# Kernel optimization log

Measured on AMD Instinct MI355X. Metric: run time of the kernel, lower is better.

## Reference

```python
import jax, jax.numpy as jnp
import numpy as np

N_ATOMS = 4096
BOX = 37.0
CUTOFF = 5.0


def _f_r(r, fe, beta, re, lam):
    # f_e * exp(-beta*(r/r_e - 1)) / (1 + (r/r_e - lamda)^20)
    x = r / re
    return fe * jnp.exp(-beta * (x - 1.0)) / (1.0 + (x - lam) ** 20)


def _phi_r(r, a, b, re, alpha, beta, kappa, lam):
    x = r / re
    l = a * jnp.exp(-alpha * (x - 1.0)) / (1.0 + (x - kappa) ** 20)
    rr = b * jnp.exp(-beta * (x - 1.0)) / (1.0 + (x - lam) ** 20)
    return l - rr


def setup_inputs() -> dict:
    key = jax.random.key(0)
    k1, k2 = jax.random.split(key)
    # coordinates in a box sized for metal-like density so neighbors exist within cutoff
    coords = jax.random.uniform(k1, (N_ATOMS, 3), dtype=jnp.float32) * BOX
    # all 22 EAM parameters positive in [1.0, 2.5] (r_e, rho_s, rho_n, rho_0, eta must be > 0)
    params = 1.0 + 1.5 * jax.random.uniform(k2, (N_ATOMS, 22), dtype=jnp.float32)
    return {"coords": coords, "params": params}


def reference(coords, params):
    N = coords.shape[0]
    # docstring column order: r_e, f_e, rho_e, rho_s, alpha, beta, A, B, kappa, lamda,
    # f_n0..f_n3, f_0..f_3, eta, f_e2, rho_n, rho_0
    r_e, f_e, rho_e, rho_s = params[:, 0], params[:, 1], params[:, 2], params[:, 3]
    alpha, beta = params[:, 4], params[:, 5]
    A, B, kappa, lam = params[:, 6], params[:, 7], params[:, 8], params[:, 9]
    eta, f_e2 = params[:, 18], params[:, 19]
    rho_n, rho_0 = params[:, 20], params[:, 21]

    # ---- full pairwise distances (safe diagonal for differentiable sqrt) ----
    diff = coords[None, :, :] - coords[:, None, :]            # [N, N, 3]
    r2 = jnp.sum(diff * diff, axis=-1)                        # [N, N]
    eye = jnp.eye(N, dtype=bool)
    r_mat = jnp.sqrt(jnp.where(eye, 1.0, r2))                 # [N, N]

    # ---- pair energy over i<j with r <= cutoff (masked, same math as torch filtering) ----
    iu, ju = jnp.triu_indices(N, k=1)                         # P = N(N-1)/2 pairs
    r_pair = r_mat[iu, ju]
    mask = r_pair <= CUTOFF
    r_safe = jnp.where(mask, r_pair, 1.0)                     # nan-safe for masked-out pairs

    fr_i = _f_r(r_safe, f_e[iu], beta[iu], r_e[iu], lam[iu])
    fr_j = _f_r(r_safe, f_e[ju], beta[ju], r_e[ju], lam[ju])
    ph_i = _phi_r(r_safe, A[iu], B[iu], r_e[iu], alpha[iu], beta[iu], kappa[iu], lam[iu])
    ph_j = _phi_r(r_safe, A[ju], B[ju], r_e[ju], alpha[ju], beta[ju], kappa[ju], lam[ju])
    phi_01 = fr_j / fr_i * ph_i + fr_i / fr_j * ph_j
    p_e = 0.5 * jnp.sum(jnp.where(mask, phi_01, 0.0))

    # ---- per-atom density rho_i = sum_{j != i} f_r(r_ij, params_j) (no cutoff, as in source) ----
    fr_mat = _f_r(r_mat, f_e[None, :], beta[None, :], r_e[None, :], lam[None, :])
    rho = jnp.sum(jnp.where(eye, 0.0, fr_mat), axis=1)        # [N]

    # ---- embedding F(rho) with three branches (if/elif/else -> nested where) ----
    xn = rho / rho_n - 1.0
    poly_n = params[:, 10] + params[:, 11] * xn + params[:, 12] * xn ** 2 + params[:, 13] * xn ** 3
    xe = rho / rho_e - 1.0
    poly_0 = params[:, 14] + params[:, 15] * xe + params[:, 16] * xe ** 2 + params[:, 17] * xe ** 3
    t = (rho / rho_s) ** eta
    tail = f_e2 * (1.0 - jnp.log(t)) * t
    F_i = jnp.where(rho < rho_n, poly_n, jnp.where(rho < rho_0, poly_0, tail))

    return p_e + jnp.sum(F_i)
```

## Files before the change

kernel.cpp:

```cpp
#include <hip/hip_runtime.h>
#include <math.h>

#define N_ATOMS 4096
#define NTILE   16
#define NJ      64
#define JT      64
#define LOG2E   1.4426950408889634f
#define LN2     0.6931471805599453f

typedef float v2f __attribute__((ext_vector_type(2)));
typedef unsigned long long u64;

__device__ __forceinline__ float pow20f(float t) {
    float t2 = t * t, t4 = t2 * t2, t8 = t4 * t4, t16 = t8 * t8;
    return t16 * t4;
}

__device__ __forceinline__ float block_reduce(float v, float* red) {
    __syncthreads();
    #pragma unroll
    for (int off = 32; off > 0; off >>= 1) v += __shfl_down(v, off, 64);
    if ((threadIdx.x & 63) == 0) red[threadIdx.x >> 6] = v;
    __syncthreads();
    return (red[0] + red[1]) + (red[2] + red[3]);
}

__global__ __launch_bounds__(256) void pack_kernel(
    const float* __restrict__ coords, const float* __restrict__ params,
    float* __restrict__ apk, float* __restrict__ rpk, int* __restrict__ ctr)
{
    if (blockIdx.x == 0 && threadIdx.x == 0) *ctr = 0;
    const int a = blockIdx.x * 256 + threadIdx.x;
    const float* p = params + 22 * a;
    const float x = coords[3*a], y = coords[3*a+1], z = coords[3*a+2];
    const float re = p[0], fe = p[1], be = p[5], al = p[4], la = p[9];
    const float rei  = __builtin_amdgcn_rcpf(re);
    const float bl2  = be * LOG2E;
    const float al2  = al * LOG2E;
    const float l2fe = __builtin_amdgcn_logf(fe);

    float lo = la + 1.0f, hi = la + 6.0f;
    #pragma unroll 1
    for (int it = 0; it < 28; ++it) {
        const float mid = 0.5f * (lo + hi);
        const float t   = mid - la;
        const float g   = l2fe - bl2 * (mid - 1.0f)
                        - __builtin_amdgcn_logf(1.0f + pow20f(t)) + 19.93f;
        if (g > 0.0f) lo = mid; else hi = mid;
    }
    const float rc  = re * hi;
    const float rc2 = fmaxf(rc * rc, 25.01f);

    float4* ad = (float4*)(apk + 12 * a);
    ad[0] = { x, y, z, rei };
    ad[1] = { -bl2 * rei, bl2 + l2fe, -la, p[7] * __builtin_amdgcn_rcpf(fe) };
    ad[2] = { -al2 * rei, al2, -p[8], p[6] };

    float* rd = rpk + 8 * (a >> 1) + (a & 1);
    rd[0] = x; rd[2] = y; rd[4] = z; rd[6] = rc2;
}

__global__ __launch_bounds__(256) void eam_main(
    const float* __restrict__ apk, const float* __restrict__ rpk,
    float* __restrict__ rho_part,
    float* __restrict__ e_part)
{
    __shared__ float4 srho4[JT];
    __shared__ float4 sphi4[JT * 3];
    __shared__ float red[4];

    const int tid = threadIdx.x;
    const int bi  = blockIdx.x;
    const int s   = blockIdx.y;
    const int i   = bi * 256 + tid;
    const int jbase = s * JT;

    if (tid < JT)       srho4[tid]      = ((const float4*)rpk)[s * JT + tid];
    else                sphi4[tid - 64] = ((const float4*)apk)[s * 192 + (tid - 64)];

    const float4* apk4 = (const float4*)apk;
    const float4 a0 = apk4[i * 3 + 0];
    const float4 a1 = apk4[i * 3 + 1];
    const float4 a2 = apk4[i * 3 + 2];

    __syncthreads();

    const v2f xi2 = { a0.x, a0.x }, yi2 = { a0.y, a0.y }, zi2 = { a0.z, a0.z };
    u64 hits = 0ull;

    #pragma unroll 4
    for (int k = 0; k < JT / 2; ++k) {
        const float4 f0 = srho4[k * 2 + 0];
        const float4 f1 = srho4[k * 2 + 1];
        const v2f x01 = { f0.x, f0.y }, y01 = { f0.z, f0.w };
        const v2f z01 = { f1.x, f1.y };
        const v2f dx = x01 - xi2, dy = y01 - yi2, dz = z01 - zi2;
        const v2f r2v = dx * dx + dy * dy + dz * dz;
        if (r2v.x <= f1.z) hits |= (1ull << (2 * k));
        if (r2v.y <= f1.w) hits |= (1ull << (2 * k + 1));
    }

    const int t = i - jbase;
    float rho = 0.0f;
    u64 phim = 0ull;

    {
        u64 m = hits;
        if (t >= 0 && t < JT) m &= ~(1ull << t);
        while (m) {
            const int k = __builtin_ctzll(m);
            m &= m - 1;
            const float4 q0 = sphi4[k * 3 + 0];
            const float4 q1 = sphi4[k * 3 + 1];
            const float dx = q0.x - a0.x, dy = q0.y - a0.y, dz = q0.z - a0.z;
            const float r2 = fmaf(dx, dx, fmaf(dy, dy, dz * dz));
            const float r  = __builtin_amdgcn_sqrtf(r2);
            const float fr = __builtin_amdgcn_exp2f(fmaf(r, q1.x, q1.y))
                           * __builtin_amdgcn_rcpf(1.0f + pow20f(fmaf(r, q0.w, q1.z)));
            rho += fr;
            if (r2 <= 25.0f && k > t) phim |= (1ull << k);
        }
    }
    rho_part[(size_t)s * N_ATOMS + i] = rho;

    float e = 0.0f;
    while (phim) {
        const int k = __builtin_ctzll(phim);
        phim &= phim - 1;
        const float4 q0 = sphi4[k * 3 + 0];
        const float4 q1 = sphi4[k * 3 + 1];
        const float4 q2 = sphi4[k * 3 + 2];
        const float dx = q0.x - a0.x, dy = q0.y - a0.y, dz = q0.z - a0.z;
        const float r = __builtin_amdgcn_sqrtf(fmaf(dx, dx, fmaf(dy, dy, dz * dz)));

        const float fri = __builtin_amdgcn_exp2f(fmaf(r, a1.x, a1.y))
                        * __builtin_amdgcn_rcpf(1.0f + pow20f(fmaf(r, a0.w, a1.z)));
        const float frj = __builtin_amdgcn_exp2f(fmaf(r, q1.x, q1.y))
                        * __builtin_amdgcn_rcpf(1.0f + pow20f(fmaf(r, q0.w, q1.z)));
        const float ph_i = a2.w * __builtin_amdgcn_exp2f(fmaf(r, a2.x, a2.y))
                                * __builtin_amdgcn_rcpf(1.0f + pow20f(fmaf(r, a0.w, a2.z)))
                         - a1.w * fri;
        const float ph_j = q2.w * __builtin_amdgcn_exp2f(fmaf(r, q2.x, q2.y))
                                * __builtin_amdgcn_rcpf(1.0f + pow20f(fmaf(r, q0.w, q2.z)))
                         - q1.w * frj;
        e += 0.5f * fmaf(frj * frj, ph_i, fri * fri * ph_j)
                  * __builtin_amdgcn_rcpf(fri * frj);
    }

    const float eb = block_reduce(e, red);
    if (tid == 0) e_part[bi * NJ + s] = eb;
}

__global__ __launch_bounds__(1024) void eam_embed(
    const float* __restrict__ params,
    const float* __restrict__ rho_part, const float* __restrict__ e_part,
    float* __restrict__ tile_sum,
    int* __restrict__ ctr, float* __restrict__ out)
{
    __shared__ float acc[4][256];
    __shared__ float red16[16];
    __shared__ int sLast;
    const int tid = threadIdx.x;
    const int b   = blockIdx.x;
    const int al  = tid & 255;
    const int q   = tid >> 8;
    const int i   = b * 256 + al;

    float part = 0.0f;
    #pragma unroll 4
    for (int s = q * 16; s < q * 16 + 16; ++s)
        part += rho_part[(size_t)s * N_ATOMS + i];
    acc[q][al] = part;
    __syncthreads();

    float v = 0.0f;
    if (tid < 256) {
        const float rhoi = (acc[0][tid] + acc[1][tid]) + (acc[2][tid] + acc[3][tid]);
        const float* p = params + 22 * i;
        float F;
        if (rhoi < p[20]) {
            const float xn = rhoi / p[20] - 1.0f;
            F = p[10] + xn * (p[11] + xn * (p[12] + xn * p[13]));
        } else if (rhoi < p[21]) {
            const float xe = rhoi / p[2] - 1.0f;
            F = p[14] + xe * (p[15] + xe * (p[16] + xe * p[17]));
        } else {
            const float l2 = __builtin_amdgcn_logf(rhoi / p[3]);
            const float tt = __builtin_amdgcn_exp2f(p[18] * l2);
            const float lt = p[18] * l2 * LN2;
            F = p[19] * (1.0f - lt) * tt;
        }
        v = F + ((tid < NJ) ? e_part[b * NJ + tid] : 0.0f);
    }

    #pragma unroll
    for (int off = 32; off > 0; off >>= 1) v += __shfl_down(v, off, 64);
    if ((tid & 63) == 0) red16[tid >> 6] = v;
    __syncthreads();
    if (tid == 0) {
        float sum = 0.0f;
        #pragma unroll
        for (int w = 0; w < 16; ++w) sum += red16[w];
        tile_sum[b] = sum;
        int prev = __hip_atomic_fetch_add(ctr, 1, __ATOMIC_ACQ_REL,
                                          __HIP_MEMORY_SCOPE_AGENT);
        sLast = (prev == NTILE - 1);
    }
    __syncthreads();

    if (sLast && tid == 0) {
        float total = 0.0f;
        #pragma unroll
        for (int w = 0; w < NTILE; ++w) total += tile_sum[w];
        out[0] = total;
    }
}

extern "C" void kernel_launch(void* const* d_in, const int* in_sizes, int n_in,
                              void* d_out, int out_size, void* d_ws, size_t ws_size,
                              hipStream_t stream) {
    const float* coords = (const float*)d_in[0];
    const float* params = (const float*)d_in[1];
    float* out = (float*)d_out;

    float* apk      = (float*)d_ws;
    float* rpk      = apk + (size_t)N_ATOMS * 12;
    float* rho_part = rpk + (size_t)(N_ATOMS / 2) * 8;
    float* e_part   = rho_part + (size_t)NJ * N_ATOMS;
    float* tile_sum = e_part + NTILE * NJ;
    int*   ctr      = (int*)(tile_sum + NTILE);

    pack_kernel<<<N_ATOMS / 256, 256, 0, stream>>>(coords, params, apk, rpk, ctr);
    dim3 grid(NTILE, NJ);
    eam_main<<<grid, 256, 0, stream>>>(apk, rpk, rho_part, e_part);
    eam_embed<<<NTILE, 1024, 0, stream>>>(params, rho_part, e_part, tile_sum, ctr, out);
}
```

Measured before the change: 23.23 us.

## Fuse parameter packing into main kernel, recomputing per-block tiles in shared memory

Removes the separate pack kernel and its workspace round trip. Each main block now computes packed parameters for its 64 j-atoms, including the 28-iteration bisection for the cutoff radius, directly into shared memory, and derives per-i constants from raw params in registers. This saves one kernel launch and a global write/read, but the bisection is recomputed redundantly in every block (16x per atom) on only 64 threads, which lengthens the prologue before the barrier.

```diff
diff --git a/kernel.cpp b/kernel.cpp
--- a/kernel.cpp
+++ b/kernel.cpp
@@ -25,45 +25,11 @@
     return (red[0] + red[1]) + (red[2] + red[3]);
 }
 
-__global__ __launch_bounds__(256) void pack_kernel(
+__global__ __launch_bounds__(256) void eam_main(
     const float* __restrict__ coords, const float* __restrict__ params,
-    float* __restrict__ apk, float* __restrict__ rpk, int* __restrict__ ctr)
-{
-    if (blockIdx.x == 0 && threadIdx.x == 0) *ctr = 0;
-    const int a = blockIdx.x * 256 + threadIdx.x;
-    const float* p = params + 22 * a;
-    const float x = coords[3*a], y = coords[3*a+1], z = coords[3*a+2];
-    const float re = p[0], fe = p[1], be = p[5], al = p[4], la = p[9];
-    const float rei  = __builtin_amdgcn_rcpf(re);
-    const float bl2  = be * LOG2E;
-    const float al2  = al * LOG2E;
-    const float l2fe = __builtin_amdgcn_logf(fe);
-
-    float lo = la + 1.0f, hi = la + 6.0f;
-    #pragma unroll 1
-    for (int it = 0; it < 28; ++it) {
-        const float mid = 0.5f * (lo + hi);
-        const float t   = mid - la;
-        const float g   = l2fe - bl2 * (mid - 1.0f)
-                        - __builtin_amdgcn_logf(1.0f + pow20f(t)) + 19.93f;
-        if (g > 0.0f) lo = mid; else hi = mid;
-    }
-    const float rc  = re * hi;
-    const float rc2 = fmaxf(rc * rc, 25.01f);
-
-    float4* ad = (float4*)(apk + 12 * a);
-    ad[0] = { x, y, z, rei };
-    ad[1] = { -bl2 * rei, bl2 + l2fe, -la, p[7] * __builtin_amdgcn_rcpf(fe) };
-    ad[2] = { -al2 * rei, al2, -p[8], p[6] };
-
-    float* rd = rpk + 8 * (a >> 1) + (a & 1);
-    rd[0] = x; rd[2] = y; rd[4] = z; rd[6] = rc2;
-}
-
-__global__ __launch_bounds__(256) void eam_main(
-    const float* __restrict__ apk, const float* __restrict__ rpk,
     float* __restrict__ rho_part,
-    float* __restrict__ e_part)
+    float* __restrict__ e_part,
+    int* __restrict__ ctr)
 {
     __shared__ float4 srho4[JT];
     __shared__ float4 sphi4[JT * 3];
@@ -75,17 +41,52 @@
     const int i   = bi * 256 + tid;
     const int jbase = s * JT;
 
-    if (tid < JT)       srho4[tid]      = ((const float4*)rpk)[s * JT + tid];
-    else                sphi4[tid - 64] = ((const float4*)apk)[s * 192 + (tid - 64)];
-
-    const float4* apk4 = (const float4*)apk;
-    const float4 a0 = apk4[i * 3 + 0];
-    const float4 a1 = apk4[i * 3 + 1];
-    const float4 a2 = apk4[i * 3 + 2];
-
-    __syncthreads();
-
-    const v2f xi2 = { a0.x, a0.x }, yi2 = { a0.y, a0.y }, zi2 = { a0.z, a0.z };
+    if (bi == 0 && s == 0 && tid == 0) *ctr = 0;
+
+    if (tid < JT) {
+        const int j = jbase + tid;
+        const float* p = params + 22 * j;
+        const float x = coords[3*j], y = coords[3*j+1], z = coords[3*j+2];
+        const float re = p[0], fe = p[1], be = p[5], al = p[4], la = p[9];
+        const float rei  = __builtin_amdgcn_rcpf(re);
+        const float bl2  = be * LOG2E;
+        const float al2  = al * LOG2E;
+        const float l2fe = __builtin_amdgcn_logf(fe);
+
+        float lo = la + 1.0f, hi = la + 6.0f;
+        #pragma unroll 1
+        for (int it = 0; it < 28; ++it) {
+            const float mid = 0.5f * (lo + hi);
+            const float g   = l2fe - bl2 * (mid - 1.0f)
+                            - __builtin_amdgcn_logf(1.0f + pow20f(mid - la)) + 19.93f;
+            if (g > 0.0f) lo = mid; else hi = mid;
+        }
+        const float rc  = re * hi;
+        const float rc2 = fmaxf(rc * rc, 25.01f);
+
+        sphi4[tid * 3 + 0] = { x, y, z, rei };
+        sphi4[tid * 3 + 1] = { -bl2 * rei, bl2 + l2fe, -la, p[7] * __builtin_amdgcn_rcpf(fe) };
+        sphi4[tid * 3 + 2] = { -al2 * rei, al2, -p[8], p[6] };
+        float* rd = (float*)srho4 + 8 * (tid >> 1) + (tid & 1);
+        rd[0] = x; rd[2] = y; rd[4] = z; rd[6] = rc2;
+    }
+
+    const float* pi = params + 22 * i;
+    const float xi = coords[3*i], yi = coords[3*i+1], zi = coords[3*i+2];
+    const float rei_i  = __builtin_amdgcn_rcpf(pi[0]);
+    const float bl2_i  = pi[5] * LOG2E;
+    const float al2_i  = pi[4] * LOG2E;
+    const float c0b_i  = -bl2_i * rei_i;
+    const float c1bp_i = bl2_i + __builtin_amdgcn_logf(pi[1]);
+    const float c0a_i  = -al2_i * rei_i;
+    const float mla_i  = -pi[9];
+    const float mka_i  = -pi[8];
+    const float A_i    = pi[6];
+    const float Bof_i  = pi[7] * __builtin_amdgcn_rcpf(pi[1]);
+
+    __syncthreads();
+
+    const v2f xi2 = { xi, xi }, yi2 = { yi, yi }, zi2 = { zi, zi };
     u64 hits = 0ull;
 
     #pragma unroll 4
@@ -112,7 +113,7 @@
             m &= m - 1;
             const float4 q0 = sphi4[k * 3 + 0];
             const float4 q1 = sphi4[k * 3 + 1];
-            const float dx = q0.x - a0.x, dy = q0.y - a0.y, dz = q0.z - a0.z;
+            const float dx = q0.x - xi, dy = q0.y - yi, dz = q0.z - zi;
             const float r2 = fmaf(dx, dx, fmaf(dy, dy, dz * dz));
             const float r  = __builtin_amdgcn_sqrtf(r2);
             const float fr = __builtin_amdgcn_exp2f(fmaf(r, q1.x, q1.y))
@@ -130,16 +131,16 @@
         const float4 q0 = sphi4[k * 3 + 0];
         const float4 q1 = sphi4[k * 3 + 1];
         const float4 q2 = sphi4[k * 3 + 2];
-        const float dx = q0.x - a0.x, dy = q0.y - a0.y, dz = q0.z - a0.z;
+        const float dx = q0.x - xi, dy = q0.y - yi, dz = q0.z - zi;
         const float r = __builtin_amdgcn_sqrtf(fmaf(dx, dx, fmaf(dy, dy, dz * dz)));
 
-        const float fri = __builtin_amdgcn_exp2f(fmaf(r, a1.x, a1.y))
-                        * __builtin_amdgcn_rcpf(1.0f + pow20f(fmaf(r, a0.w, a1.z)));
+        const float fri = __builtin_amdgcn_exp2f(fmaf(r, c0b_i, c1bp_i))
+                        * __builtin_amdgcn_rcpf(1.0f + pow20f(fmaf(r, rei_i, mla_i)));
         const float frj = __builtin_amdgcn_exp2f(fmaf(r, q1.x, q1.y))
                         * __builtin_amdgcn_rcpf(1.0f + pow20f(fmaf(r, q0.w, q1.z)));
-        const float ph_i = a2.w * __builtin_amdgcn_exp2f(fmaf(r, a2.x, a2.y))
-                                * __builtin_amdgcn_rcpf(1.0f + pow20f(fmaf(r, a0.w, a2.z)))
-                         - a1.w * fri;
+        const float ph_i = A_i * __builtin_amdgcn_exp2f(fmaf(r, c0a_i, al2_i))
+                               * __builtin_amdgcn_rcpf(1.0f + pow20f(fmaf(r, rei_i, mka_i)))
+                         - Bof_i * fri;
         const float ph_j = q2.w * __builtin_amdgcn_exp2f(fmaf(r, q2.x, q2.y))
                                 * __builtin_amdgcn_rcpf(1.0f + pow20f(fmaf(r, q0.w, q2.z)))
                          - q1.w * frj;
@@ -223,15 +224,12 @@
     const float* params = (const float*)d_in[1];
     float* out = (float*)d_out;
 
-    float* apk      = (float*)d_ws;
-    float* rpk      = apk + (size_t)N_ATOMS * 12;
-    float* rho_part = rpk + (size_t)(N_ATOMS / 2) * 8;
+    float* rho_part = (float*)d_ws;
     float* e_part   = rho_part + (size_t)NJ * N_ATOMS;
     float* tile_sum = e_part + NTILE * NJ;
     int*   ctr      = (int*)(tile_sum + NTILE);
 
-    pack_kernel<<<N_ATOMS / 256, 256, 0, stream>>>(coords, params, apk, rpk, ctr);
     dim3 grid(NTILE, NJ);
-    eam_main<<<grid, 256, 0, stream>>>(apk, rpk, rho_part, e_part);
+    eam_main<<<grid, 256, 0, stream>>>(coords, params, rho_part, e_part, ctr);
     eam_embed<<<NTILE, 1024, 0, stream>>>(params, rho_part, e_part, tile_sum, ctr, out);
 }
```

New measurement: 20.22 us. 13.0% less time.
